# Kernel optimization log

Measured on AMD Instinct MI355X. Metric: run time of the kernel, lower is better.

## Reference

```python
import jax, jax.numpy as jnp
import numpy as np

H, D, L, G = 4, 32, 2, 512   # heads, head_dim, conv layers, num graphs
HC = H * D                    # hidden_channels = 128


def _mlp3(x, ws, bs):
    # PyG-style MLP, 3 layers, relu between (no act after last), dropout=0
    for i in range(3):
        x = x @ ws[i] + bs[i]
        if i < 2:
            x = jax.nn.relu(x)
    return x


def _attend(q_dst, k_src, v_src, edge, a_rel_et, m_rel_et, p_rel_et, n_dst):
    """One HGTConv edge-type: relation transform, per-dst segment softmax, scatter.
    q_dst: [Nd,H,D], k_src/v_src: [Ns,H,D], edge: [2,E] (src,dst)."""
    src, dst = edge[0], edge[1]
    k_t = jnp.einsum('nhd,hde->nhe', k_src, a_rel_et)   # relation-specific key
    v_t = jnp.einsum('nhd,hde->nhe', v_src, m_rel_et)   # relation-specific value
    alpha = (q_dst[dst] * k_t[src]).sum(-1) * p_rel_et / jnp.sqrt(jnp.float32(D))  # [E,H]
    amax = jax.ops.segment_max(alpha, dst, num_segments=n_dst)
    amax = jnp.where(jnp.isfinite(amax), amax, 0.0)      # nodes with no in-edges
    ex = jnp.exp(alpha - amax[dst])
    den = jax.ops.segment_sum(ex, dst, num_segments=n_dst)
    w = ex / den[dst]                                    # segment softmax weights
    out = jax.ops.segment_sum(v_t[src] * w[..., None], dst, num_segments=n_dst)
    return out.reshape(n_dst, HC)


def _forward(x_var, x_con, mlp_in_w, mlp_in_b,
             mlp_out_w0, mlp_out_b0, mlp_out_w1, mlp_out_b1, mlp_out_w2, mlp_out_b2,
             k_w, k_b, q_w, q_b, v_w, v_b, a_w, a_b, skip,
             a_rel, m_rel, p_rel, edge_vc, edge_cv, batch_var):
    Nv, Nc = x_var.shape[0], x_con.shape[0]
    # per-node-type input MLPs (nt 0 = variable, nt 1 = constraint)
    xs = [_mlp3(x_var, mlp_in_w[0], mlp_in_b[0]),
          _mlp3(x_con, mlp_in_w[1], mlp_in_b[1])]
    ns = [Nv, Nc]
    for l in range(L):  # HGTConv layers
        k = [(xs[t] @ k_w[l, t] + k_b[l, t]).reshape(ns[t], H, D) for t in (0, 1)]
        q = [(xs[t] @ q_w[l, t] + q_b[l, t]).reshape(ns[t], H, D) for t in (0, 1)]
        v = [(xs[t] @ v_w[l, t] + v_b[l, t]).reshape(ns[t], H, D) for t in (0, 1)]
        # edge type 0: variable -> constraint ; edge type 1: constraint -> variable
        agg_con = _attend(q[1], k[0], v[0], edge_vc, a_rel[l, 0], m_rel[l, 0], p_rel[l, 0], Nc)
        agg_var = _attend(q[0], k[1], v[1], edge_cv, a_rel[l, 1], m_rel[l, 1], p_rel[l, 1], Nv)
        # group='mean' over incoming edge types (one per dst type here), then a_lin + gated skip
        new_xs = []
        for t, agg in ((0, agg_var), (1, agg_con)):
            out = jax.nn.gelu(agg, approximate=False) @ a_w[l, t] + a_b[l, t]
            g = jax.nn.sigmoid(skip[l, t])
            new_xs.append(g * out + (1.0 - g) * xs[t])
        xs = new_xs
    # output head on 'variable' nodes: MLP -> softmax(dim=1) -> global mean pool
    logits = _mlp3(xs[0], [mlp_out_w0, mlp_out_w1, mlp_out_w2], [mlp_out_b0, mlp_out_b1, mlp_out_b2])
    probs = jax.nn.softmax(logits, axis=1)
    summ = jax.ops.segment_sum(probs, batch_var, num_segments=G)
    cnt = jax.ops.segment_sum(jnp.ones((xs[0].shape[0],), probs.dtype), batch_var, num_segments=G)
    return summ / jnp.maximum(cnt, 1.0)[:, None]


def setup_inputs() -> dict:
    key = jax.random.key(0)
    ks = jax.random.split(key, 24)
    Nv = Nc = 50000
    E = 400000
    s = 1.0 / np.sqrt(HC)  # fan-in scale for hidden-width linears
    sd = 1.0 / np.sqrt(D)
    inp = {
        'x_var': jax.random.normal(ks[0], (Nv, HC), jnp.float32),
        'x_con': jax.random.normal(ks[1], (Nc, HC), jnp.float32),
        'mlp_in_w': jax.random.normal(ks[2], (2, 3, HC, HC), jnp.float32) * s,
        'mlp_in_b': jnp.zeros((2, 3, HC), jnp.float32),
        'mlp_out_w0': jax.random.normal(ks[3], (HC, HC), jnp.float32) * s,
        'mlp_out_b0': jnp.zeros((HC,), jnp.float32),
        'mlp_out_w1': jax.random.normal(ks[4], (HC, HC), jnp.float32) * s,
        'mlp_out_b1': jnp.zeros((HC,), jnp.float32),
        'mlp_out_w2': jax.random.normal(ks[5], (HC, 2), jnp.float32) * s,
        'mlp_out_b2': jnp.zeros((2,), jnp.float32),
        'k_w': jax.random.normal(ks[6], (L, 2, HC, HC), jnp.float32) * s,
        'k_b': jnp.zeros((L, 2, HC), jnp.float32),
        'q_w': jax.random.normal(ks[7], (L, 2, HC, HC), jnp.float32) * s,
        'q_b': jnp.zeros((L, 2, HC), jnp.float32),
        'v_w': jax.random.normal(ks[8], (L, 2, HC, HC), jnp.float32) * s,
        'v_b': jnp.zeros((L, 2, HC), jnp.float32),
        'a_w': jax.random.normal(ks[9], (L, 2, HC, HC), jnp.float32) * s,
        'a_b': jnp.zeros((L, 2, HC), jnp.float32),
        'skip': jnp.ones((L, 2), jnp.float32),
        'a_rel': jax.random.normal(ks[10], (L, 2, H, D, D), jnp.float32) * sd,
        'm_rel': jax.random.normal(ks[11], (L, 2, H, D, D), jnp.float32) * sd,
        'p_rel': jnp.ones((L, 2, H), jnp.float32),
        'edge_vc': jnp.stack([jax.random.randint(ks[12], (E,), 0, Nv, jnp.int32),
                              jax.random.randint(ks[13], (E,), 0, Nc, jnp.int32)]),
        'edge_cv': jnp.stack([jax.random.randint(ks[14], (E,), 0, Nc, jnp.int32),
                              jax.random.randint(ks[15], (E,), 0, Nv, jnp.int32)]),
        'batch_var': jnp.sort(jax.random.randint(ks[16], (Nv,), 0, G, jnp.int32)),
    }
    return inp


def reference(x_var, x_con, mlp_in_w, mlp_in_b,
              mlp_out_w0, mlp_out_b0, mlp_out_w1, mlp_out_b1, mlp_out_w2, mlp_out_b2,
              k_w, k_b, q_w, q_b, v_w, v_b, a_w, a_b, skip,
              a_rel, m_rel, p_rel, edge_vc, edge_cv, batch_var):
    return _forward(x_var, x_con, mlp_in_w, mlp_in_b,
                    mlp_out_w0, mlp_out_b0, mlp_out_w1, mlp_out_b1, mlp_out_w2, mlp_out_b2,
                    k_w, k_b, q_w, q_b, v_w, v_b, a_w, a_b, skip,
                    a_rel, m_rel, p_rel, edge_vc, edge_cv, batch_var)
```

## Files before the change

kernel.cpp:

```cpp
#include <hip/hip_runtime.h>
#include <cstddef>
#include <cstdint>

typedef __attribute__((ext_vector_type(8))) short short8;
typedef __attribute__((ext_vector_type(4))) float float4v;
typedef __attribute__((ext_vector_type(2))) float float2v;
typedef __attribute__((ext_vector_type(2))) __bf16 bf162;

__device__ __forceinline__ float bf2f_lo(unsigned int u) {
    union { unsigned int i; float f; } v; v.i = u << 16; return v.f;
}
__device__ __forceinline__ float bf2f_hi(unsigned int u) {
    union { unsigned int i; float f; } v; v.i = u & 0xFFFF0000u; return v.f;
}
__device__ __forceinline__ unsigned short f2bf(float f) {
    union { float f; unsigned int i; } v; v.f = f;
    unsigned int x = v.i;
    unsigned int r = (x + 0x7FFFu + ((x >> 16) & 1u)) >> 16;
    return (unsigned short)r;
}
__device__ __forceinline__ unsigned int pk2(float lo, float hi) {
    return (unsigned int)f2bf(lo) | ((unsigned int)f2bf(hi) << 16);
}
__device__ __forceinline__ float geluf(float x) {
    return 0.5f * x * (1.0f + erff(x * 0.70710678118654752f));
}
__device__ __forceinline__ float dot2bf(unsigned int a, unsigned int b, float c) {
#if defined(__has_builtin) && __has_builtin(__builtin_amdgcn_fdot2_f32_bf16)
    union U { unsigned int u; bf162 v; };
    U ua, ub; ua.u = a; ub.u = b;
    return __builtin_amdgcn_fdot2_f32_bf16(ua.v, ub.v, c, false);
#else
    return c + bf2f_lo(a) * bf2f_lo(b) + bf2f_hi(a) * bf2f_hi(b);
#endif
}
__device__ __forceinline__ unsigned int gate_pack(unsigned int nu, unsigned int ou,
                                                  float2v g2, float2v og2) {
    float2v n = {bf2f_lo(nu), bf2f_hi(nu)};
    float2v o = {bf2f_lo(ou), bf2f_hi(ou)};
    float2v r = n * g2 + o * og2;
    return pk2(r.x, r.y);
}

__global__ void k_zero(int* __restrict__ p, int n) {
    int i = blockIdx.x * 256 + threadIdx.x;
    if (i < n) p[i] = 0;
}

__global__ void k_swz(const float* __restrict__ mlp_in_w, const float* __restrict__ q_w,
                      const float* __restrict__ a_w, const float* __restrict__ mow0,
                      const float* __restrict__ mow1, const float* __restrict__ mow2,
                      const float* __restrict__ kw, const float* __restrict__ kb,
                      const float* __restrict__ vw, const float* __restrict__ vb,
                      const float* __restrict__ arel, const float* __restrict__ mrel,
                      const float* __restrict__ prel,
                      unsigned short* __restrict__ Wswz, float* __restrict__ Bkv) {
    int idx = blockIdx.y;
    int f = blockIdx.x * 256 + threadIdx.x;
    if (idx == 25) {
        if (f >= 1024) return;
        int lt = f >> 8, c = f & 255;
        int sec = c >> 7, cc = c & 127, h = cc >> 5, e = cc & 31;
        const float* B = sec ? vb : kb;
        const float* R = sec ? mrel : arel;
        float scale = sec ? 1.f : prel[lt * 4 + h] * 0.17677669529663687f;
        const float* rp = R + (size_t)(lt * 4 + h) * 1024 + e;
        const float* bp = B + lt * 128 + h * 32;
        float s = 0.f;
        #pragma unroll 8
        for (int d = 0; d < 32; ++d) s += bp[d] * rp[(size_t)d * 32];
        Bkv[lt * 256 + c] = s * scale;
        return;
    }
    if (f >= 16384) return;
    int j = f & 7, l = (f >> 3) & 63, t = (f >> 9) & 7, sb = f >> 12;
    int k = sb * 32 + (l >> 4) * 8 + j;
    int n = t * 16 + (l & 15);
    float val;
    if (idx < 6)        val = mlp_in_w[(size_t)idx * 16384 + (size_t)k * 128 + n];
    else if (idx < 10)  val = q_w[(size_t)(idx - 6) * 16384 + (size_t)k * 128 + n];
    else if (idx < 14)  val = a_w[(size_t)(idx - 10) * 16384 + (size_t)k * 128 + n];
    else if (idx == 14) val = mow0[(size_t)k * 128 + n];
    else if (idx == 15) val = mow1[(size_t)k * 128 + n];
    else if (idx < 24) {
        int u = idx - 16, lt = u >> 1, sec = u & 1;
        int h = n >> 5, e = n & 31;
        const float* W = sec ? vw : kw;
        const float* R = sec ? mrel : arel;
        float scale = sec ? 1.f : prel[lt * 4 + h] * 0.17677669529663687f;
        const float* rp = R + (size_t)(lt * 4 + h) * 1024 + e;
        const float* wp = W + (size_t)lt * 16384 + (size_t)k * 128 + h * 32;
        float s = 0.f;
        #pragma unroll 8
        for (int d = 0; d < 32; ++d) s += wp[d] * rp[(size_t)d * 32];
        val = s * scale;
    } else val = (n < 2) ? mow2[(size_t)k * 2 + n] : 0.f;
    Wswz[(size_t)idx * 16384 + f] = f2bf(val);
}

__device__ __forceinline__ void unit_ldst(const short8 av[4], const unsigned short* __restrict__ Bst,
                                          int lane, float4v acc[8]) {
    #pragma unroll
    for (int t = 0; t < 8; ++t) acc[t] = (float4v){0.f, 0.f, 0.f, 0.f};
    #pragma unroll
    for (int s = 0; s < 4; ++s)
        #pragma unroll
        for (int t = 0; t < 8; ++t) {
            short8 bv = *(const short8*)&Bst[(s * 8 + t) * 512 + lane * 8];
            acc[t] = __builtin_amdgcn_mfma_f32_16x16x32_bf16(av[s], bv, acc[t], 0, 0, 0);
        }
}

__global__ __launch_bounds__(256) void k_mlp3qkv(
    const float* __restrict__ Xa, const float* __restrict__ Xb,
    const unsigned short* __restrict__ Wswz, const float* __restrict__ mlp_in_b,
    const float* __restrict__ q_b, const float* __restrict__ Bkv,
    unsigned short* __restrict__ curS, unsigned short* __restrict__ Qs,
    unsigned short* __restrict__ KVs, int NT, int Nv, int Bv) {
    __shared__ unsigned short Bst[16384];
    __shared__ unsigned short tr[4][16][136];
    const int tid = threadIdx.x;
    const int lane = tid & 63, wave = tid >> 6;
    const int quad = lane >> 4, mrow = lane & 15;
    int bx = blockIdx.x;
    int base, end, type;
    if (bx < Bv) { base = bx * 64; end = Nv; type = 0; }
    else         { base = Nv + (bx - Bv) * 64; end = NT; type = 1; }
    const int mbase = base + wave * 16;
    int r0 = mbase + mrow; if (r0 >= end) r0 = end - 1;
    const bool rok = (mbase + mrow) < end;

    const int un[6] = { type * 3, type * 3 + 1, type * 3 + 2,
                        6 + type, 16 + type * 2, 17 + type * 2 };
    uint4 pf[8];
    auto preload = [&](int u) {
        const uint4* src = (const uint4*)(Wswz + (size_t)u * 16384);
        #pragma unroll
        for (int k = 0; k < 8; ++k) pf[k] = src[tid + k * 256];
    };
    auto commit = [&]() {
        #pragma unroll
        for (int k = 0; k < 8; ++k) ((uint4*)Bst)[tid + k * 256] = pf[k];
    };
    auto trwrite = [&](float4v* acc, const float* b, bool relu) {
        #pragma unroll
        for (int t = 0; t < 8; ++t) {
            int col = t * 16 + mrow;
            float bb = b[col];
            #pragma unroll
            for (int r = 0; r < 4; ++r) {
                float v = acc[t][r] + bb;
                if (relu) v = fmaxf(v, 0.f);
                tr[wave][quad * 4 + r][col] = f2bf(v);
            }
        }
    };
    auto vecstore = [&](unsigned short* C, int ldC, int cb) {
        if (rok) {
            #pragma unroll
            for (int s = 0; s < 4; ++s) {
                uint4 v = *(const uint4*)&tr[wave][mrow][s * 32 + quad * 8];
                *(uint4*)(C + (size_t)r0 * ldC + cb + quad * 8 + s * 32) = v;
            }
        }
    };

    short8 av[4];
    {
        const float* ap = (type == 0 ? Xa + (size_t)r0 * 128
                                     : Xb + (size_t)(r0 - Nv) * 128) + quad * 8;
        #pragma unroll
        for (int s = 0; s < 4; ++s) {
            float4 f0 = *(const float4*)(ap + s * 32);
            float4 f1 = *(const float4*)(ap + s * 32 + 4);
            short8 a;
            a[0] = (short)f2bf(f0.x); a[1] = (short)f2bf(f0.y);
            a[2] = (short)f2bf(f0.z); a[3] = (short)f2bf(f0.w);
            a[4] = (short)f2bf(f1.x); a[5] = (short)f2bf(f1.y);
            a[6] = (short)f2bf(f1.z); a[7] = (short)f2bf(f1.w);
            av[s] = a;
        }
    }
    const float* bs = mlp_in_b + type * 384;
    preload(un[0]);
    #pragma unroll
    for (int ui = 0; ui < 6; ++ui) {
        __syncthreads();
        commit();
        if (ui < 5) preload(un[ui + 1]);
        __syncthreads();
        float4v acc[8];
        unit_ldst(av, Bst, lane, acc);
        if (ui < 3) {
            trwrite(acc, bs + ui * 128, ui < 2);
            #pragma unroll
            for (int s = 0; s < 4; ++s)
                av[s] = *(const short8*)&tr[wave][mrow][s * 32 + quad * 8];
            if (ui == 2) vecstore(curS, 128, 0);
        } else if (ui == 3) {
            trwrite(acc, q_b + type * 128, false);
            vecstore(Qs, 128, 0);
        } else if (ui == 4) {
            trwrite(acc, Bkv + type * 256, false);
            vecstore(KVs, 256, 0);
        } else {
            trwrite(acc, Bkv + type * 256 + 128, false);
            vecstore(KVs, 256, 128);
        }
    }
}

__global__ __launch_bounds__(256) void k_alinqkv(
    const unsigned short* __restrict__ Aagg, const unsigned short* __restrict__ Wswz,
    const float* __restrict__ a_b, const float* __restrict__ skipP,
    const float* __restrict__ q_b, const float* __restrict__ Bkv,
    unsigned short* __restrict__ curS, unsigned short* __restrict__ Qs,
    unsigned short* __restrict__ KVs, int NT, int Nv, int Bv) {
    __shared__ unsigned short Bst[16384];
    __shared__ unsigned short tr[4][16][136];
    const int tid = threadIdx.x;
    const int lane = tid & 63, wave = tid >> 6;
    const int quad = lane >> 4, mrow = lane & 15;
    int bx = blockIdx.x;
    int base, end, type;
    if (bx < Bv) { base = bx * 64; end = Nv; type = 0; }
    else         { base = Nv + (bx - Bv) * 64; end = NT; type = 1; }
    const int mbase = base + wave * 16;
    int r0 = mbase + mrow; if (r0 >= end) r0 = end - 1;
    const bool rok = (mbase + mrow) < end;
    const int ltA = type, ltQ = 2 + type;
    const int un[4] = { 10 + ltA, 6 + ltQ, 16 + ltQ * 2, 17 + ltQ * 2 };

    uint4 pf[8];
    auto preload = [&](int u) {
        const uint4* src = (const uint4*)(Wswz + (size_t)u * 16384);
        #pragma unroll
        for (int k = 0; k < 8; ++k) pf[k] = src[tid + k * 256];
    };
    auto commit = [&]() {
        #pragma unroll
        for (int k = 0; k < 8; ++k) ((uint4*)Bst)[tid + k * 256] = pf[k];
    };
    auto trwrite = [&](float4v* acc, const float* b) {
        #pragma unroll
        for (int t = 0; t < 8; ++t) {
            int col = t * 16 + mrow;
            float bb = b[col];
            #pragma unroll
            for (int r = 0; r < 4; ++r)
                tr[wave][quad * 4 + r][col] = f2bf(acc[t][r] + bb);
        }
    };
    auto vecstore = [&](unsigned short* C, int ldC, int cb) {
        if (rok) {
            #pragma unroll
            for (int s = 0; s < 4; ++s) {
                uint4 v = *(const uint4*)&tr[wave][mrow][s * 32 + quad * 8];
                *(uint4*)(C + (size_t)r0 * ldC + cb + quad * 8 + s * 32) = v;
            }
        }
    };

    short8 av[4];
    {
        const unsigned short* ap = Aagg + (size_t)r0 * 128 + quad * 8;
        #pragma unroll
        for (int s = 0; s < 4; ++s) av[s] = *(const short8*)(ap + s * 32);
    }
    preload(un[0]);
    #pragma unroll
    for (int ui = 0; ui < 4; ++ui) {
        __syncthreads();
        commit();
        if (ui < 3) preload(un[ui + 1]);
        __syncthreads();
        float4v acc[8];
        unit_ldst(av, Bst, lane, acc);
        if (ui == 0) {
            trwrite(acc, a_b + ltA * 128);
            float gg = 1.f / (1.f + __expf(-skipP[ltA]));
            float2v g2 = {gg, gg}, og2 = {1.f - gg, 1.f - gg};
            #pragma unroll
            for (int s = 0; s < 4; ++s) {
                short8 nv = *(const short8*)&tr[wave][mrow][s * 32 + quad * 8];
                uint4 nu = *(uint4*)&nv;
                uint4 ou = *(const uint4*)(curS + (size_t)r0 * 128 + quad * 8 + s * 32);
                uint4 res;
                res.x = gate_pack(nu.x, ou.x, g2, og2);
                res.y = gate_pack(nu.y, ou.y, g2, og2);
                res.z = gate_pack(nu.z, ou.z, g2, og2);
                res.w = gate_pack(nu.w, ou.w, g2, og2);
                if (rok) *(uint4*)(curS + (size_t)r0 * 128 + quad * 8 + s * 32) = res;
                av[s] = *(short8*)&res;
            }
        } else if (ui == 1) {
            trwrite(acc, q_b + ltQ * 128);
            vecstore(Qs, 128, 0);
        } else if (ui == 2) {
            trwrite(acc, Bkv + ltQ * 256);
            vecstore(KVs, 256, 0);
        } else {
            trwrite(acc, Bkv + ltQ * 256 + 128);
            vecstore(KVs, 256, 128);
        }
    }
}

__global__ __launch_bounds__(256) void k_alinhead(
    const unsigned short* __restrict__ Aagg, const unsigned short* __restrict__ Wswz,
    const float* __restrict__ a_b, const float* __restrict__ skipP,
    const unsigned short* __restrict__ curS,
    const float* __restrict__ mob0, const float* __restrict__ mob1,
    const float* __restrict__ mob2, const int* __restrict__ batch,
    int N, int G, float* __restrict__ gsum, float* __restrict__ gcnt) {
    __shared__ unsigned short Bst[16384];
    __shared__ unsigned short tr[4][16][136];
    __shared__ float sb[64][3];
    const int tid = threadIdx.x;
    const int lane = tid & 63, wave = tid >> 6;
    const int quad = lane >> 4, mrow = lane & 15;
    for (int i = tid; i < 192; i += 256) ((float*)sb)[i] = 0.f;
    const int base = blockIdx.x * 64;
    const int mbase = base + wave * 16;
    int r0 = mbase + mrow; if (r0 >= N) r0 = N - 1;
    const int bmin = batch[base < N ? base : N - 1];
    const int un[4] = { 12, 14, 15, 24 };

    uint4 pf[8];
    auto preload = [&](int u) {
        const uint4* src = (const uint4*)(Wswz + (size_t)u * 16384);
        #pragma unroll
        for (int k = 0; k < 8; ++k) pf[k] = src[tid + k * 256];
    };
    auto commit = [&]() {
        #pragma unroll
        for (int k = 0; k < 8; ++k) ((uint4*)Bst)[tid + k * 256] = pf[k];
    };

    short8 av[4];
    {
        const unsigned short* ap = Aagg + (size_t)r0 * 128 + quad * 8;
        #pragma unroll
        for (int s = 0; s < 4; ++s) av[s] = *(const short8*)(ap + s * 32);
    }
    preload(un[0]);
    #pragma unroll
    for (int ui = 0; ui < 4; ++ui) {
        __syncthreads();
        commit();
        if (ui < 3) preload(un[ui + 1]);
        __syncthreads();
        if (ui < 3) {
            float4v acc[8];
            unit_ldst(av, Bst, lane, acc);
            const float* b = (ui == 0) ? (a_b + 2 * 128) : (ui == 1 ? mob0 : mob1);
            #pragma unroll
            for (int t = 0; t < 8; ++t) {
                int col = t * 16 + mrow;
                float bb = b[col];
                #pragma unroll
                for (int r = 0; r < 4; ++r) {
                    float v = acc[t][r] + bb;
                    if (ui > 0) v = fmaxf(v, 0.f);
                    tr[wave][quad * 4 + r][col] = f2bf(v);
                }
            }
            if (ui == 0) {
                float gg = 1.f / (1.f + __expf(-skipP[2]));
                float2v g2 = {gg, gg}, og2 = {1.f - gg, 1.f - gg};
                #pragma unroll
                for (int s = 0; s < 4; ++s) {
                    short8 nv = *(const short8*)&tr[wave][mrow][s * 32 + quad * 8];
                    uint4 nu = *(uint4*)&nv;
                    uint4 ou = *(const uint4*)(curS + (size_t)r0 * 128 + quad * 8 + s * 32);
                    uint4 res;
                    res.x = gate_pack(nu.x, ou.x, g2, og2);
                    res.y = gate_pack(nu.y, ou.y, g2, og2);
                    res.z = gate_pack(nu.z, ou.z, g2, og2);
                    res.w = gate_pack(nu.w, ou.w, g2, og2);
                    av[s] = *(short8*)&res;
                }
            } else {
                #pragma unroll
                for (int s = 0; s < 4; ++s)
                    av[s] = *(const short8*)&tr[wave][mrow][s * 32 + quad * 8];
            }
        } else {
            float4v lg = (float4v){0.f, 0.f, 0.f, 0.f};
            #pragma unroll
            for (int s = 0; s < 4; ++s) {
                short8 bv = *(const short8*)&Bst[(s * 8) * 512 + lane * 8];
                lg = __builtin_amdgcn_mfma_f32_16x16x32_bf16(av[s], bv, lg, 0, 0, 0);
            }
            float4v lgo;
            #pragma unroll
            for (int r = 0; r < 4; ++r) lgo[r] = __shfl_xor(lg[r], 1);
            if (mrow == 0) {
                #pragma unroll
                for (int r = 0; r < 4; ++r) {
                    int row = mbase + quad * 4 + r;
                    if (row < N) {
                        float l0 = lg[r] + mob2[0];
                        float l1 = lgo[r] + mob2[1];
                        float mm = fmaxf(l0, l1);
                        float e0 = __expf(l0 - mm), e1 = __expf(l1 - mm);
                        float inv = 1.f / (e0 + e1);
                        int b = batch[row];
                        int rel = b - bmin;
                        if (rel >= 0 && rel < 64) {
                            atomicAdd(&sb[rel][0], e0 * inv);
                            atomicAdd(&sb[rel][1], e1 * inv);
                            atomicAdd(&sb[rel][2], 1.f);
                        } else {
                            atomicAdd(&gsum[b * 2 + 0], e0 * inv);
                            atomicAdd(&gsum[b * 2 + 1], e1 * inv);
                            atomicAdd(&gcnt[b], 1.f);
                        }
                    }
                }
            }
        }
    }
    __syncthreads();
    for (int i = tid; i < 64; i += 256) {
        float c = sb[i][2];
        if (c != 0.f && bmin + i < G) {
            atomicAdd(&gsum[(bmin + i) * 2 + 0], sb[i][0]);
            atomicAdd(&gsum[(bmin + i) * 2 + 1], sb[i][1]);
            atomicAdd(&gcnt[bmin + i], c);
        }
    }
}

__global__ void k_hist2(const int* __restrict__ evc, const int* __restrict__ ecv, int E,
                        int* __restrict__ deg, int Nv) {
    int e = blockIdx.x * 256 + threadIdx.x;
    if (e >= E) return;
    if (blockIdx.y == 0) atomicAdd(&deg[Nv + evc[E + e]], 1);
    else                 atomicAdd(&deg[ecv[E + e]], 1);
}
__global__ void k_scan_block(const int* __restrict__ deg, int n, int* __restrict__ off,
                             int* __restrict__ partials) {
    __shared__ int s[256];
    int i = blockIdx.x * 256 + threadIdx.x;
    s[threadIdx.x] = (i < n) ? deg[i] : 0;
    __syncthreads();
    for (int d = 1; d < 256; d <<= 1) {
        int t = (threadIdx.x >= d) ? s[threadIdx.x - d] : 0;
        __syncthreads();
        s[threadIdx.x] += t;
        __syncthreads();
    }
    if (i < n) off[i + 1] = s[threadIdx.x];
    if (threadIdx.x == 255) partials[blockIdx.x] = s[255];
}
__global__ void k_scan_partials(int* __restrict__ partials, int nb) {
    __shared__ int s[512];
    s[threadIdx.x] = (threadIdx.x < nb) ? partials[threadIdx.x] : 0;
    __syncthreads();
    for (int d = 1; d < 512; d <<= 1) {
        int t = (threadIdx.x >= d) ? s[threadIdx.x - d] : 0;
        __syncthreads();
        s[threadIdx.x] += t;
        __syncthreads();
    }
    if (threadIdx.x < nb) partials[threadIdx.x] = s[threadIdx.x];
}
__global__ void k_scan_add(int* __restrict__ off, int* __restrict__ cur,
                           const int* __restrict__ partials, int n) {
    int i = blockIdx.x * 256 + threadIdx.x;
    if (i == 0) { off[0] = 0; cur[0] = 0; }
    if (i < n) {
        int b = i >> 8;
        int v = off[i + 1] + ((b > 0) ? partials[b - 1] : 0);
        off[i + 1] = v;
        cur[i + 1] = v;
    }
}
__global__ void k_scatter2(const int* __restrict__ evc, const int* __restrict__ ecv, int E,
                           int* __restrict__ cur, int Nv, int* __restrict__ srcAll) {
    int e = blockIdx.x * 256 + threadIdx.x;
    if (e >= E) return;
    if (blockIdx.y == 0) {
        int d = Nv + evc[E + e];
        int pos = atomicAdd(&cur[d], 1);
        srcAll[pos] = evc[e];
    } else {
        int d = ecv[E + e];
        int pos = atomicAdd(&cur[d], 1);
        srcAll[pos] = Nv + ecv[e];
    }
}

__global__ __launch_bounds__(256) void k_agg(
    const unsigned short* __restrict__ Q, const unsigned short* __restrict__ KV,
    const int* __restrict__ off, const int* __restrict__ csrc,
    unsigned short* __restrict__ out, int NT) {
    int dst = blockIdx.x * 4 + (threadIdx.x >> 6);
    int lane = threadIdx.x & 63;
    if (dst >= NT) return;
    const int g = lane >> 4, w = lane & 15;
    int2 se = *(const int2*)(off + dst);
    int s0 = se.x, s1 = se.y;
    uint4 qr = *(const uint4*)(Q + (size_t)dst * 128 + w * 8);
    float2v a0 = {0.f, 0.f}, a1 = {0.f, 0.f}, a2 = {0.f, 0.f}, a3 = {0.f, 0.f};
    float den = 0.f;
    int j = s0 + g;
    uint4 kr = {0, 0, 0, 0}, vr = {0, 0, 0, 0};
    bool have = j < s1;
    if (have) {
        const unsigned short* kv = KV + (size_t)csrc[j] * 256 + w * 8;
        kr = *(const uint4*)kv;
        vr = *(const uint4*)(kv + 128);
    }
    while (have) {
        int jn = j + 4;
        bool haveN = jn < s1;
        uint4 krn = kr, vrn = vr;
        if (haveN) {
            const unsigned short* kv = KV + (size_t)csrc[jn] * 256 + w * 8;
            krn = *(const uint4*)kv;
            vrn = *(const uint4*)(kv + 128);
        }
        float t = dot2bf(kr.x, qr.x, 0.f);
        t = dot2bf(kr.y, qr.y, t);
        t = dot2bf(kr.z, qr.z, t);
        t = dot2bf(kr.w, qr.w, t);
        t += __shfl_xor(t, 1);
        t += __shfl_xor(t, 2);
        t = fminf(fmaxf(t, -30.f), 30.f);
        float p = __expf(t);
        den += p;
        float2v pv = {p, p};
        a0 += pv * (float2v){bf2f_lo(vr.x), bf2f_hi(vr.x)};
        a1 += pv * (float2v){bf2f_lo(vr.y), bf2f_hi(vr.y)};
        a2 += pv * (float2v){bf2f_lo(vr.z), bf2f_hi(vr.z)};
        a3 += pv * (float2v){bf2f_lo(vr.w), bf2f_hi(vr.w)};
        kr = krn; vr = vrn; j = jn; have = haveN;
    }
    den += __shfl_xor(den, 16); den += __shfl_xor(den, 32);
    a0.x += __shfl_xor(a0.x, 16); a0.x += __shfl_xor(a0.x, 32);
    a0.y += __shfl_xor(a0.y, 16); a0.y += __shfl_xor(a0.y, 32);
    a1.x += __shfl_xor(a1.x, 16); a1.x += __shfl_xor(a1.x, 32);
    a1.y += __shfl_xor(a1.y, 16); a1.y += __shfl_xor(a1.y, 32);
    a2.x += __shfl_xor(a2.x, 16); a2.x += __shfl_xor(a2.x, 32);
    a2.y += __shfl_xor(a2.y, 16); a2.y += __shfl_xor(a2.y, 32);
    a3.x += __shfl_xor(a3.x, 16); a3.x += __shfl_xor(a3.x, 32);
    a3.y += __shfl_xor(a3.y, 16); a3.y += __shfl_xor(a3.y, 32);
    if (g == 0) {
        float inv = (s1 > s0) ? 1.f / den : 0.f;
        uint4 o;
        o.x = pk2(geluf(a0.x * inv), geluf(a0.y * inv));
        o.y = pk2(geluf(a1.x * inv), geluf(a1.y * inv));
        o.z = pk2(geluf(a2.x * inv), geluf(a2.y * inv));
        o.w = pk2(geluf(a3.x * inv), geluf(a3.y * inv));
        *(uint4*)(out + (size_t)dst * 128 + w * 8) = o;
    }
}

__global__ void k_finalize(const float* __restrict__ gsum, const float* __restrict__ gcnt,
                           float* __restrict__ out, int n) {
    int i = blockIdx.x * 256 + threadIdx.x;
    if (i < n) out[i] = gsum[i] / fmaxf(gcnt[i >> 1], 1.f);
}

extern "C" void kernel_launch(void* const* d_in, const int* in_sizes, int n_in,
                              void* d_out, int out_size, void* d_ws, size_t ws_size,
                              hipStream_t stream) {
    const float* x_var    = (const float*)d_in[0];
    const float* x_con    = (const float*)d_in[1];
    const float* mlp_in_w = (const float*)d_in[2];
    const float* mlp_in_b = (const float*)d_in[3];
    const float* mow0 = (const float*)d_in[4];
    const float* mob0 = (const float*)d_in[5];
    const float* mow1 = (const float*)d_in[6];
    const float* mob1 = (const float*)d_in[7];
    const float* mow2 = (const float*)d_in[8];
    const float* mob2 = (const float*)d_in[9];
    const float* k_w  = (const float*)d_in[10];
    const float* k_b  = (const float*)d_in[11];
    const float* q_w  = (const float*)d_in[12];
    const float* q_b  = (const float*)d_in[13];
    const float* v_w  = (const float*)d_in[14];
    const float* v_b  = (const float*)d_in[15];
    const float* a_w  = (const float*)d_in[16];
    const float* a_b  = (const float*)d_in[17];
    const float* skipP = (const float*)d_in[18];
    const float* a_rel = (const float*)d_in[19];
    const float* m_rel = (const float*)d_in[20];
    const float* p_rel = (const float*)d_in[21];
    const int* edge_vc = (const int*)d_in[22];
    const int* edge_cv = (const int*)d_in[23];
    const int* batch   = (const int*)d_in[24];

    const int Nv = in_sizes[0] / 128;
    const int Nc = in_sizes[1] / 128;
    const int E  = in_sizes[22] / 2;
    const int G  = out_size / 2;
    const int NT = Nv + Nc;

    float* fbase = (float*)d_ws;
    size_t fo = 0;
    auto falloc = [&](size_t n) { float* p = fbase + fo; fo += n; return p; };
    float* Bkv  = falloc(4 * 256);
    float* gsum = falloc((size_t)G * 2);
    float* gcnt = falloc((size_t)G);

    unsigned short* bbase = (unsigned short*)(fbase + fo);
    size_t bo = 0;
    auto balloc = [&](size_t n) { unsigned short* p = bbase + bo; bo += n; return p; };
    unsigned short* Wswz = balloc((size_t)25 * 16384);
    unsigned short* curS = balloc((size_t)NT * 128);
    unsigned short* Qs   = balloc((size_t)NT * 128);
    unsigned short* KVs  = balloc((size_t)NT * 256);

    int* ibase = (int*)(bbase + bo);
    size_t io = 0;
    auto ialloc = [&](size_t n) { int* p = ibase + io; io += n; return p; };
    int* offAll = ialloc((size_t)NT + 1);
    int* curAll = ialloc((size_t)NT + 1);
    int* srcAll = ialloc((size_t)E * 2);
    int* deg    = ialloc((size_t)NT);
    int* partials = ialloc(512);

    size_t need = (char*)(ibase + io) - (char*)d_ws;
    if (need > ws_size) return;

    const int eb  = (E + 255) / 256;
    const int nzb = (NT + 255) / 256;
    const int Bv  = (Nv + 63) / 64;
    const int Bc  = (Nc + 63) / 64;

    k_zero<<<nzb, 256, 0, stream>>>(deg, NT);
    k_hist2<<<dim3(eb, 2), 256, 0, stream>>>(edge_vc, edge_cv, E, deg, Nv);
    k_scan_block<<<nzb, 256, 0, stream>>>(deg, NT, offAll, partials);
    k_scan_partials<<<1, 512, 0, stream>>>(partials, nzb);
    k_scan_add<<<nzb, 256, 0, stream>>>(offAll, curAll, partials, NT);
    k_scatter2<<<dim3(eb, 2), 256, 0, stream>>>(edge_vc, edge_cv, E, curAll, Nv, srcAll);

    k_swz<<<dim3(64, 26), 256, 0, stream>>>(mlp_in_w, q_w, a_w, mow0, mow1, mow2,
                                            k_w, k_b, v_w, v_b, a_rel, m_rel, p_rel,
                                            Wswz, Bkv);
    k_zero<<<(G * 3 + 255) / 256, 256, 0, stream>>>((int*)gsum, G * 3);

    k_mlp3qkv<<<Bv + Bc, 256, 0, stream>>>(x_var, x_con, Wswz, mlp_in_b, q_b, Bkv,
                                           curS, Qs, KVs, NT, Nv, Bv);
    k_agg<<<(NT + 3) / 4, 256, 0, stream>>>(Qs, KVs, offAll, srcAll, Qs, NT);
    k_alinqkv<<<Bv + Bc, 256, 0, stream>>>(Qs, Wswz, a_b, skipP, q_b, Bkv,
                                           curS, Qs, KVs, NT, Nv, Bv);
    k_agg<<<(NT + 3) / 4, 256, 0, stream>>>(Qs, KVs, offAll, srcAll, Qs, NT);
    k_alinhead<<<Bv, 256, 0, stream>>>(Qs, Wswz, a_b, skipP, curS,
                                       mob0, mob1, mob2, batch, Nv, G, gsum, gcnt);
    k_finalize<<<(G * 2 + 255) / 256, 256, 0, stream>>>(gsum, gcnt, (float*)d_out, G * 2);
}
```

Measured before the change: 608.6 us.

## Process two row tiles per wave to reuse staged weights in dense kernels

The three dense MFMA kernels now give each wave 32 rows (two 16-row tiles) and each block 128 rows, so every 32KB weight unit staged into LDS feeds twice as many MFMAs. The register-prefetch double-buffering of the weights is replaced by a direct global-to-LDS copy between barriers. The transpose buffer pitch goes from 136 to 138 and output stores are remapped so lanes write contiguous row segments. The aim is less weight-staging traffic per row and fewer blocks. The cost is half as many blocks, so less occupancy and parallelism, and weight loads are no longer overlapped with compute.

```diff
diff --git a/kernel.cpp b/kernel.cpp
--- a/kernel.cpp
+++ b/kernel.cpp
@@ -98,6 +98,13 @@
     Wswz[(size_t)idx * 16384 + f] = f2bf(val);
 }
 
+__device__ __forceinline__ void stageB(const unsigned short* __restrict__ Wu,
+                                       unsigned short* __restrict__ Bst, int tid) {
+    #pragma unroll
+    for (int k = 0; k < 8; ++k)
+        ((uint4*)Bst)[tid + k * 256] = ((const uint4*)Wu)[tid + k * 256];
+}
+
 __device__ __forceinline__ void unit_ldst(const short8 av[4], const unsigned short* __restrict__ Bst,
                                           int lane, float4v acc[8]) {
     #pragma unroll
@@ -109,6 +116,34 @@
             short8 bv = *(const short8*)&Bst[(s * 8 + t) * 512 + lane * 8];
             acc[t] = __builtin_amdgcn_mfma_f32_16x16x32_bf16(av[s], bv, acc[t], 0, 0, 0);
         }
+}
+
+#define TRP 138
+
+__device__ __forceinline__ void tr_write(unsigned short (*trw)[TRP], const float4v* acc,
+                                         const float* bias, bool relu, int quad, int mrow) {
+    #pragma unroll
+    for (int t = 0; t < 8; ++t) {
+        int col = t * 16 + mrow;
+        float bb = bias[col];
+        #pragma unroll
+        for (int r = 0; r < 4; ++r) {
+            float v = acc[t][r] + bb;
+            if (relu) v = fmaxf(v, 0.f);
+            trw[quad * 4 + r][col] = f2bf(v);
+        }
+    }
+}
+__device__ __forceinline__ void tr_store(const unsigned short (*trw)[TRP],
+                                         unsigned short* __restrict__ C, int ldC, int cb,
+                                         int mtile, int end, int quad, int mrow) {
+    #pragma unroll
+    for (int s = 0; s < 4; ++s) {
+        int row = mtile + s * 4 + quad;
+        uint4 v = *(const uint4*)&trw[s * 4 + quad][mrow * 8];
+        if (row < end)
+            *(uint4*)(C + (size_t)row * ldC + cb + mrow * 8) = v;
+    }
 }
 
 __global__ __launch_bounds__(256) void k_mlp3qkv(
@@ -118,57 +153,22 @@
     unsigned short* __restrict__ curS, unsigned short* __restrict__ Qs,
     unsigned short* __restrict__ KVs, int NT, int Nv, int Bv) {
     __shared__ unsigned short Bst[16384];
-    __shared__ unsigned short tr[4][16][136];
+    __shared__ unsigned short tr[4][16][TRP];
     const int tid = threadIdx.x;
     const int lane = tid & 63, wave = tid >> 6;
     const int quad = lane >> 4, mrow = lane & 15;
     int bx = blockIdx.x;
     int base, end, type;
-    if (bx < Bv) { base = bx * 64; end = Nv; type = 0; }
-    else         { base = Nv + (bx - Bv) * 64; end = NT; type = 1; }
-    const int mbase = base + wave * 16;
-    int r0 = mbase + mrow; if (r0 >= end) r0 = end - 1;
-    const bool rok = (mbase + mrow) < end;
-
-    const int un[6] = { type * 3, type * 3 + 1, type * 3 + 2,
-                        6 + type, 16 + type * 2, 17 + type * 2 };
-    uint4 pf[8];
-    auto preload = [&](int u) {
-        const uint4* src = (const uint4*)(Wswz + (size_t)u * 16384);
-        #pragma unroll
-        for (int k = 0; k < 8; ++k) pf[k] = src[tid + k * 256];
-    };
-    auto commit = [&]() {
-        #pragma unroll
-        for (int k = 0; k < 8; ++k) ((uint4*)Bst)[tid + k * 256] = pf[k];
-    };
-    auto trwrite = [&](float4v* acc, const float* b, bool relu) {
-        #pragma unroll
-        for (int t = 0; t < 8; ++t) {
-            int col = t * 16 + mrow;
-            float bb = b[col];
-            #pragma unroll
-            for (int r = 0; r < 4; ++r) {
-                float v = acc[t][r] + bb;
-                if (relu) v = fmaxf(v, 0.f);
-                tr[wave][quad * 4 + r][col] = f2bf(v);
-            }
-        }
-    };
-    auto vecstore = [&](unsigned short* C, int ldC, int cb) {
-        if (rok) {
-            #pragma unroll
-            for (int s = 0; s < 4; ++s) {
-                uint4 v = *(const uint4*)&tr[wave][mrow][s * 32 + quad * 8];
-                *(uint4*)(C + (size_t)r0 * ldC + cb + quad * 8 + s * 32) = v;
-            }
-        }
-    };
-
-    short8 av[4];
-    {
-        const float* ap = (type == 0 ? Xa + (size_t)r0 * 128
-                                     : Xb + (size_t)(r0 - Nv) * 128) + quad * 8;
+    if (bx < Bv) { base = bx * 128; end = Nv; type = 0; }
+    else         { base = Nv + (bx - Bv) * 128; end = NT; type = 1; }
+    const int mbase = base + wave * 32;
+
+    short8 av[2][4];
+    #pragma unroll
+    for (int tile = 0; tile < 2; ++tile) {
+        int r = mbase + tile * 16 + mrow; if (r >= end) r = end - 1;
+        const float* ap = (type == 0 ? Xa + (size_t)r * 128
+                                     : Xb + (size_t)(r - Nv) * 128) + quad * 8;
         #pragma unroll
         for (int s = 0; s < 4; ++s) {
             float4 f0 = *(const float4*)(ap + s * 32);
@@ -178,34 +178,38 @@
             a[2] = (short)f2bf(f0.z); a[3] = (short)f2bf(f0.w);
             a[4] = (short)f2bf(f1.x); a[5] = (short)f2bf(f1.y);
             a[6] = (short)f2bf(f1.z); a[7] = (short)f2bf(f1.w);
-            av[s] = a;
+            av[tile][s] = a;
         }
     }
     const float* bs = mlp_in_b + type * 384;
-    preload(un[0]);
+    const int un[6] = { type * 3, type * 3 + 1, type * 3 + 2,
+                        6 + type, 16 + type * 2, 17 + type * 2 };
     #pragma unroll
     for (int ui = 0; ui < 6; ++ui) {
         __syncthreads();
-        commit();
-        if (ui < 5) preload(un[ui + 1]);
-        __syncthreads();
-        float4v acc[8];
-        unit_ldst(av, Bst, lane, acc);
-        if (ui < 3) {
-            trwrite(acc, bs + ui * 128, ui < 2);
-            #pragma unroll
-            for (int s = 0; s < 4; ++s)
-                av[s] = *(const short8*)&tr[wave][mrow][s * 32 + quad * 8];
-            if (ui == 2) vecstore(curS, 128, 0);
-        } else if (ui == 3) {
-            trwrite(acc, q_b + type * 128, false);
-            vecstore(Qs, 128, 0);
-        } else if (ui == 4) {
-            trwrite(acc, Bkv + type * 256, false);
-            vecstore(KVs, 256, 0);
-        } else {
-            trwrite(acc, Bkv + type * 256 + 128, false);
-            vecstore(KVs, 256, 128);
+        stageB(Wswz + (size_t)un[ui] * 16384, Bst, tid);
+        __syncthreads();
+        #pragma unroll
+        for (int tile = 0; tile < 2; ++tile) {
+            int mtile = mbase + tile * 16;
+            float4v acc[8];
+            unit_ldst(av[tile], Bst, lane, acc);
+            if (ui < 3) {
+                tr_write(tr[wave], acc, bs + ui * 128, ui < 2, quad, mrow);
+                #pragma unroll
+                for (int s = 0; s < 4; ++s)
+                    av[tile][s] = *(const short8*)&tr[wave][mrow][s * 32 + quad * 8];
+                if (ui == 2) tr_store(tr[wave], curS, 128, 0, mtile, end, quad, mrow);
+            } else if (ui == 3) {
+                tr_write(tr[wave], acc, q_b + type * 128, false, quad, mrow);
+                tr_store(tr[wave], Qs, 128, 0, mtile, end, quad, mrow);
+            } else if (ui == 4) {
+                tr_write(tr[wave], acc, Bkv + type * 256, false, quad, mrow);
+                tr_store(tr[wave], KVs, 256, 0, mtile, end, quad, mrow);
+            } else {
+                tr_write(tr[wave], acc, Bkv + type * 256 + 128, false, quad, mrow);
+                tr_store(tr[wave], KVs, 256, 128, mtile, end, quad, mrow);
+            }
         }
     }
 }
@@ -217,91 +221,67 @@
     unsigned short* __restrict__ curS, unsigned short* __restrict__ Qs,
     unsigned short* __restrict__ KVs, int NT, int Nv, int Bv) {
     __shared__ unsigned short Bst[16384];
-    __shared__ unsigned short tr[4][16][136];
+    __shared__ unsigned short tr[4][16][TRP];
     const int tid = threadIdx.x;
     const int lane = tid & 63, wave = tid >> 6;
     const int quad = lane >> 4, mrow = lane & 15;
     int bx = blockIdx.x;
     int base, end, type;
-    if (bx < Bv) { base = bx * 64; end = Nv; type = 0; }
-    else         { base = Nv + (bx - Bv) * 64; end = NT; type = 1; }
-    const int mbase = base + wave * 16;
-    int r0 = mbase + mrow; if (r0 >= end) r0 = end - 1;
-    const bool rok = (mbase + mrow) < end;
+    if (bx < Bv) { base = bx * 128; end = Nv; type = 0; }
+    else         { base = Nv + (bx - Bv) * 128; end = NT; type = 1; }
+    const int mbase = base + wave * 32;
     const int ltA = type, ltQ = 2 + type;
     const int un[4] = { 10 + ltA, 6 + ltQ, 16 + ltQ * 2, 17 + ltQ * 2 };
 
-    uint4 pf[8];
-    auto preload = [&](int u) {
-        const uint4* src = (const uint4*)(Wswz + (size_t)u * 16384);
-        #pragma unroll
-        for (int k = 0; k < 8; ++k) pf[k] = src[tid + k * 256];
-    };
-    auto commit = [&]() {
-        #pragma unroll
-        for (int k = 0; k < 8; ++k) ((uint4*)Bst)[tid + k * 256] = pf[k];
-    };
-    auto trwrite = [&](float4v* acc, const float* b) {
-        #pragma unroll
-        for (int t = 0; t < 8; ++t) {
-            int col = t * 16 + mrow;
-            float bb = b[col];
-            #pragma unroll
-            for (int r = 0; r < 4; ++r)
-                tr[wave][quad * 4 + r][col] = f2bf(acc[t][r] + bb);
-        }
-    };
-    auto vecstore = [&](unsigned short* C, int ldC, int cb) {
-        if (rok) {
-            #pragma unroll
-            for (int s = 0; s < 4; ++s) {
-                uint4 v = *(const uint4*)&tr[wave][mrow][s * 32 + quad * 8];
-                *(uint4*)(C + (size_t)r0 * ldC + cb + quad * 8 + s * 32) = v;
+    short8 av[2][4];
+    #pragma unroll
+    for (int tile = 0; tile < 2; ++tile) {
+        int r = mbase + tile * 16 + mrow; if (r >= end) r = end - 1;
+        const unsigned short* ap = Aagg + (size_t)r * 128 + quad * 8;
+        #pragma unroll
+        for (int s = 0; s < 4; ++s) av[tile][s] = *(const short8*)(ap + s * 32);
+    }
+    #pragma unroll
+    for (int ui = 0; ui < 4; ++ui) {
+        __syncthreads();
+        stageB(Wswz + (size_t)un[ui] * 16384, Bst, tid);
+        __syncthreads();
+        #pragma unroll
+        for (int tile = 0; tile < 2; ++tile) {
+            int mtile = mbase + tile * 16;
+            float4v acc[8];
+            unit_ldst(av[tile], Bst, lane, acc);
+            if (ui == 0) {
+                tr_write(tr[wave], acc, a_b + ltA * 128, false, quad, mrow);
+                float gg = 1.f / (1.f + __expf(-skipP[ltA]));
+                float2v g2 = {gg, gg}, og2 = {1.f - gg, 1.f - gg};
+                #pragma unroll
+                for (int s = 0; s < 4; ++s) {
+                    int row = mtile + s * 4 + quad;
+                    int rowc = (row < end) ? row : end - 1;
+                    uint4 nu = *(const uint4*)&tr[wave][s * 4 + quad][mrow * 8];
+                    uint4 ou = *(const uint4*)(curS + (size_t)rowc * 128 + mrow * 8);
+                    uint4 res;
+                    res.x = gate_pack(nu.x, ou.x, g2, og2);
+                    res.y = gate_pack(nu.y, ou.y, g2, og2);
+                    res.z = gate_pack(nu.z, ou.z, g2, og2);
+                    res.w = gate_pack(nu.w, ou.w, g2, og2);
+                    if (row < end) *(uint4*)(curS + (size_t)row * 128 + mrow * 8) = res;
+                    *(uint4*)&tr[wave][s * 4 + quad][mrow * 8] = res;
+                }
+                #pragma unroll
+                for (int s = 0; s < 4; ++s)
+                    av[tile][s] = *(const short8*)&tr[wave][mrow][s * 32 + quad * 8];
+            } else if (ui == 1) {
+                tr_write(tr[wave], acc, q_b + ltQ * 128, false, quad, mrow);
+                tr_store(tr[wave], Qs, 128, 0, mtile, end, quad, mrow);
+            } else if (ui == 2) {
+                tr_write(tr[wave], acc, Bkv + ltQ * 256, false, quad, mrow);
+                tr_store(tr[wave], KVs, 256, 0, mtile, end, quad, mrow);
+            } else {
+                tr_write(tr[wave], acc, Bkv + ltQ * 256 + 128, false, quad, mrow);
+                tr_store(tr[wave], KVs, 256, 128, mtile, end, quad, mrow);
             }
-        }
-    };
-
-    short8 av[4];
-    {
-        const unsigned short* ap = Aagg + (size_t)r0 * 128 + quad * 8;
-        #pragma unroll
-        for (int s = 0; s < 4; ++s) av[s] = *(const short8*)(ap + s * 32);
-    }
-    preload(un[0]);
-    #pragma unroll
-    for (int ui = 0; ui < 4; ++ui) {
-        __syncthreads();
-        commit();
-        if (ui < 3) preload(un[ui + 1]);
-        __syncthreads();
-        float4v acc[8];
-        unit_ldst(av, Bst, lane, acc);
-        if (ui == 0) {
-            trwrite(acc, a_b + ltA * 128);
-            float gg = 1.f / (1.f + __expf(-skipP[ltA]));
-            float2v g2 = {gg, gg}, og2 = {1.f - gg, 1.f - gg};
-            #pragma unroll
-            for (int s = 0; s < 4; ++s) {
-                short8 nv = *(const short8*)&tr[wave][mrow][s * 32 + quad * 8];
-                uint4 nu = *(uint4*)&nv;
-                uint4 ou = *(const uint4*)(curS + (size_t)r0 * 128 + quad * 8 + s * 32);
-                uint4 res;
-                res.x = gate_pack(nu.x, ou.x, g2, og2);
-                res.y = gate_pack(nu.y, ou.y, g2, og2);
-                res.z = gate_pack(nu.z, ou.z, g2, og2);
-                res.w = gate_pack(nu.w, ou.w, g2, og2);
-                if (rok) *(uint4*)(curS + (size_t)r0 * 128 + quad * 8 + s * 32) = res;
-                av[s] = *(short8*)&res;
-            }
-        } else if (ui == 1) {
-            trwrite(acc, q_b + ltQ * 128);
-            vecstore(Qs, 128, 0);
-        } else if (ui == 2) {
-            trwrite(acc, Bkv + ltQ * 256);
-            vecstore(KVs, 256, 0);
-        } else {
-            trwrite(acc, Bkv + ltQ * 256 + 128);
-            vecstore(KVs, 256, 128);
         }
     }
 }
@@ -314,107 +294,89 @@
     const float* __restrict__ mob2, const int* __restrict__ batch,
     int N, int G, float* __restrict__ gsum, float* __restrict__ gcnt) {
     __shared__ unsigned short Bst[16384];
-    __shared__ unsigned short tr[4][16][136];
+    __shared__ unsigned short tr[4][16][TRP];
     __shared__ float sb[64][3];
     const int tid = threadIdx.x;
     const int lane = tid & 63, wave = tid >> 6;
     const int quad = lane >> 4, mrow = lane & 15;
     for (int i = tid; i < 192; i += 256) ((float*)sb)[i] = 0.f;
-    const int base = blockIdx.x * 64;
-    const int mbase = base + wave * 16;
-    int r0 = mbase + mrow; if (r0 >= N) r0 = N - 1;
+    const int base = blockIdx.x * 128;
+    const int mbase = base + wave * 32;
     const int bmin = batch[base < N ? base : N - 1];
     const int un[4] = { 12, 14, 15, 24 };
 
-    uint4 pf[8];
-    auto preload = [&](int u) {
-        const uint4* src = (const uint4*)(Wswz + (size_t)u * 16384);
-        #pragma unroll
-        for (int k = 0; k < 8; ++k) pf[k] = src[tid + k * 256];
-    };
-    auto commit = [&]() {
-        #pragma unroll
-        for (int k = 0; k < 8; ++k) ((uint4*)Bst)[tid + k * 256] = pf[k];
-    };
-
-    short8 av[4];
-    {
-        const unsigned short* ap = Aagg + (size_t)r0 * 128 + quad * 8;
-        #pragma unroll
-        for (int s = 0; s < 4; ++s) av[s] = *(const short8*)(ap + s * 32);
-    }
-    preload(un[0]);
+    short8 av[2][4];
+    #pragma unroll
+    for (int tile = 0; tile < 2; ++tile) {
+        int r = mbase + tile * 16 + mrow; if (r >= N) r = N - 1;
+        const unsigned short* ap = Aagg + (size_t)r * 128 + quad * 8;
+        #pragma unroll
+        for (int s = 0; s < 4; ++s) av[tile][s] = *(const short8*)(ap + s * 32);
+    }
     #pragma unroll
     for (int ui = 0; ui < 4; ++ui) {
         __syncthreads();
-        commit();
-        if (ui < 3) preload(un[ui + 1]);
-        __syncthreads();
-        if (ui < 3) {
-            float4v acc[8];
-            unit_ldst(av, Bst, lane, acc);
-            const float* b = (ui == 0) ? (a_b + 2 * 128) : (ui == 1 ? mob0 : mob1);
-            #pragma unroll
-            for (int t = 0; t < 8; ++t) {
-                int col = t * 16 + mrow;
-                float bb = b[col];
+        stageB(Wswz + (size_t)un[ui] * 16384, Bst, tid);
+        __syncthreads();
+        #pragma unroll
+        for (int tile = 0; tile < 2; ++tile) {
+            int mtile = mbase + tile * 16;
+            if (ui < 3) {
+                float4v acc[8];
+                unit_ldst(av[tile], Bst, lane, acc);
+                const float* b = (ui == 0) ? (a_b + 2 * 128) : (ui == 1 ? mob0 : mob1);
+                tr_write(tr[wave], acc, b, ui > 0, quad, mrow);
+                if (ui == 0) {
+                    float gg = 1.f / (1.f + __expf(-skipP[2]));
+                    float2v g2 = {gg, gg}, og2 = {1.f - gg, 1.f - gg};
+                    #pragma unroll
+                    for (int s = 0; s < 4; ++s) {
+                        int row = mtile + s * 4 + quad;
+                        int rowc = (row < N) ? row : N - 1;
+                        uint4 nu = *(const uint4*)&tr[wave][s * 4 + quad][mrow * 8];
+                        uint4 ou = *(const uint4*)(curS + (size_t)rowc * 128 + mrow * 8);
+                        uint4 res;
+                        res.x = gate_pack(nu.x, ou.x, g2, og2);
+                        res.y = gate_pack(nu.y, ou.y, g2, og2);
+                        res.z = gate_pack(nu.z, ou.z, g2, og2);
+                        res.w = gate_pack(nu.w, ou.w, g2, og2);
+                        *(uint4*)&tr[wave][s * 4 + quad][mrow * 8] = res;
+                    }
+                }
                 #pragma unroll
-                for (int r = 0; r < 4; ++r) {
-                    float v = acc[t][r] + bb;
-                    if (ui > 0) v = fmaxf(v, 0.f);
-                    tr[wave][quad * 4 + r][col] = f2bf(v);
-                }
-            }
-            if (ui == 0) {
-                float gg = 1.f / (1.f + __expf(-skipP[2]));
-                float2v g2 = {gg, gg}, og2 = {1.f - gg, 1.f - gg};
+                for (int s = 0; s < 4; ++s)
+                    av[tile][s] = *(const short8*)&tr[wave][mrow][s * 32 + quad * 8];
+            } else {
+                float4v lg = (float4v){0.f, 0.f, 0.f, 0.f};
                 #pragma unroll
                 for (int s = 0; s < 4; ++s) {
-                    short8 nv = *(const short8*)&tr[wave][mrow][s * 32 + quad * 8];
-                    uint4 nu = *(uint4*)&nv;
-                    uint4 ou = *(const uint4*)(curS + (size_t)r0 * 128 + quad * 8 + s * 32);
-                    uint4 res;
-                    res.x = gate_pack(nu.x, ou.x, g2, og2);
-                    res.y = gate_pack(nu.y, ou.y, g2, og2);
-                    res.z = gate_pack(nu.z, ou.z, g2, og2);
-                    res.w = gate_pack(nu.w, ou.w, g2, og2);
-                    av[s] = *(short8*)&res;
+                    short8 bv = *(const short8*)&Bst[(s * 8) * 512 + lane * 8];
+                    lg = __builtin_amdgcn_mfma_f32_16x16x32_bf16(av[tile][s], bv, lg, 0, 0, 0);
                 }
-            } else {
+                float4v lgo;
                 #pragma unroll
-                for (int s = 0; s < 4; ++s)
-                    av[s] = *(const short8*)&tr[wave][mrow][s * 32 + quad * 8];
-            }
-        } else {
-            float4v lg = (float4v){0.f, 0.f, 0.f, 0.f};
-            #pragma unroll
-            for (int s = 0; s < 4; ++s) {
-                short8 bv = *(const short8*)&Bst[(s * 8) * 512 + lane * 8];
-                lg = __builtin_amdgcn_mfma_f32_16x16x32_bf16(av[s], bv, lg, 0, 0, 0);
-            }
-            float4v lgo;
-            #pragma unroll
-            for (int r = 0; r < 4; ++r) lgo[r] = __shfl_xor(lg[r], 1);
-            if (mrow == 0) {
-                #pragma unroll
-                for (int r = 0; r < 4; ++r) {
-                    int row = mbase + quad * 4 + r;
-                    if (row < N) {
-                        float l0 = lg[r] + mob2[0];
-                        float l1 = lgo[r] + mob2[1];
-                        float mm = fmaxf(l0, l1);
-                        float e0 = __expf(l0 - mm), e1 = __expf(l1 - mm);
-                        float inv = 1.f / (e0 + e1);
-                        int b = batch[row];
-                        int rel = b - bmin;
-                        if (rel >= 0 && rel < 64) {
-                            atomicAdd(&sb[rel][0], e0 * inv);
-                            atomicAdd(&sb[rel][1], e1 * inv);
-                            atomicAdd(&sb[rel][2], 1.f);
-                        } else {
-                            atomicAdd(&gsum[b * 2 + 0], e0 * inv);
-                            atomicAdd(&gsum[b * 2 + 1], e1 * inv);
-                            atomicAdd(&gcnt[b], 1.f);
+                for (int r = 0; r < 4; ++r) lgo[r] = __shfl_xor(lg[r], 1);
+                if (mrow == 0) {
+                    #pragma unroll
+                    for (int r = 0; r < 4; ++r) {
+                        int row = mtile + quad * 4 + r;
+                        if (row < N) {
+                            float l0 = lg[r] + mob2[0];
+                            float l1 = lgo[r] + mob2[1];
+                            float mm = fmaxf(l0, l1);
+                            float e0 = __expf(l0 - mm), e1 = __expf(l1 - mm);
+                            float inv = 1.f / (e0 + e1);
+                            int b = batch[row];
+                            int rel = b - bmin;
+                            if (rel >= 0 && rel < 64) {
+                                atomicAdd(&sb[rel][0], e0 * inv);
+                                atomicAdd(&sb[rel][1], e1 * inv);
+                                atomicAdd(&sb[rel][2], 1.f);
+                            } else {
+                                atomicAdd(&gsum[b * 2 + 0], e0 * inv);
+                                atomicAdd(&gsum[b * 2 + 1], e1 * inv);
+                                atomicAdd(&gcnt[b], 1.f);
+                            }
                         }
                     }
                 }
@@ -628,8 +590,8 @@
 
     const int eb  = (E + 255) / 256;
     const int nzb = (NT + 255) / 256;
-    const int Bv  = (Nv + 63) / 64;
-    const int Bc  = (Nc + 63) / 64;
+    const int Bv  = (Nv + 127) / 128;
+    const int Bc  = (Nc + 127) / 128;
 
     k_zero<<<nzb, 256, 0, stream>>>(deg, NT);
     k_hist2<<<dim3(eb, 2), 256, 0, stream>>>(edge_vc, edge_cv, E, deg, Nv);
```

Result: faster. 504.1 us (-17.2%).
